# Kernel optimization log

Measured on AMD Instinct MI355X. Metric: run time of the kernel, lower is better.

The kernel has to match this reference:

```python
import jax, jax.numpy as jnp
import numpy as np

# dims
B, L, D0, P, K = 4, 512, 640, 128, 16
C, H, NL = 32, 4, 3            # hidden channels, heads, layers
DH = C // H
RAD_IN = P + 2                 # pair feat + bppm + distance
HPT = 0.3                      # high_prob_threshold


def _build_edges(bppm, coords):
    """Backbone + kNN + high-prob edges per sample, deduped, flattened over batch."""
    src_all, dst_all = [], []
    for b in range(B):
        s_bb = np.arange(L - 1); d_bb = np.arange(1, L)
        srcs = [s_bb, d_bb]; dsts = [d_bb, s_bb]
        c = coords[b]
        d2 = ((c[:, None, :] - c[None, :, :]) ** 2).sum(-1)
        nn = np.argsort(d2, axis=1)[:, 1:K + 1]            # exclude self
        s_knn = np.repeat(np.arange(L), K); d_knn = nn.reshape(-1)
        srcs += [s_knn, d_knn]; dsts += [d_knn, s_knn]
        iu, ju = np.triu_indices(L, 2)                      # |i-j| > 1
        m = bppm[b][iu, ju] >= HPT
        hs, hd = iu[m], ju[m]
        srcs += [hs, hd]; dsts += [hd, hs]
        e = np.unique(np.stack([np.concatenate(srcs), np.concatenate(dsts)], 1), axis=0)
        src_all.append(e[:, 0] + b * L); dst_all.append(e[:, 1] + b * L)
    return np.concatenate(src_all).astype(np.int32), np.concatenate(dst_all).astype(np.int32)


def setup_inputs() -> dict:
    rng = np.random.default_rng(0)
    sequence_rep = rng.standard_normal((B, L, D0)).astype(np.float32)
    pair_rep = rng.standard_normal((B, L, L, P)).astype(np.float32)
    u = rng.random((B, L, L)).astype(np.float32)
    bppm = (0.5 * (u + u.transpose(0, 2, 1))) ** 8          # sparse-ish symmetric BPPM
    initial_coords = (10.0 * rng.standard_normal((B, L, 3))).astype(np.float32)
    edge_src, edge_dst = _build_edges(bppm, initial_coords)

    def w(*shape):
        fan = shape[-2] if len(shape) >= 2 else shape[-1]
        return (rng.standard_normal(shape) / np.sqrt(fan)).astype(np.float32)

    inp = dict(
        sequence_rep=jnp.asarray(sequence_rep), pair_rep=jnp.asarray(pair_rep),
        bppm=jnp.asarray(bppm.astype(np.float32)), initial_coords=jnp.asarray(initial_coords),
        edge_src=jnp.asarray(edge_src), edge_dst=jnp.asarray(edge_dst),
        Win0=jnp.asarray(w(D0, C)), Win1=jnp.asarray(w(1, C)),
        Wr1=jnp.asarray(w(NL, RAD_IN, 64)), br1=jnp.zeros((NL, 64), jnp.float32),
        Wr2=jnp.asarray(w(NL, 64, 4 * C)), br2=jnp.zeros((NL, 4 * C), jnp.float32),
        Wm00=jnp.asarray(w(NL, C, C)), Wm01=jnp.asarray(w(NL, C, C)),
        Wm10=jnp.asarray(w(NL, C, C)), Wm11=jnp.asarray(w(NL, C, C)),
        Wq=jnp.asarray(w(NL, C, C)), Wself0=jnp.asarray(w(NL, C, C)), Wself1=jnp.asarray(w(NL, C, C)),
        gamma0=jnp.ones((NL, C), jnp.float32), beta0=jnp.zeros((NL, C), jnp.float32),
        gamma1=jnp.ones((NL, C), jnp.float32), Wout=jnp.asarray(w(C, 1)),
    )
    return inp


def _forward(sequence_rep, pair_rep, bppm, initial_coords,
             Win0, Win1, Wr1, br1, Wr2, br2, Wm00, Wm01, Wm10, Wm11,
             Wq, Wself0, Wself1, gamma0, beta0, gamma1, Wout, edge_src, edge_dst):
    N = B * L
    x = initial_coords.reshape(N, 3)
    h0 = sequence_rep.reshape(N, D0) @ Win0                  # [N,C] degree-0
    h1 = x[:, None, :] * Win1[0][None, :, None]              # [N,C,3] degree-1
    src, dst = edge_src, edge_dst
    rel = x[dst] - x[src]
    r = jnp.sqrt(jnp.sum(rel * rel, -1) + 1e-12)             # [E]
    rhat = rel / (r[:, None] + 1e-8)                         # Y1 spherical harmonic dir
    b_idx, si, di = src // L, src % L, dst % L
    ef = jnp.concatenate([pair_rep[b_idx, si, di], bppm[b_idx, si, di][:, None], r[:, None]], -1)

    for l in range(NL):
        rad = jax.nn.relu(ef @ Wr1[l] + br1[l]) @ Wr2[l] + br2[l]   # [E,4C] radial weights
        w00, w01, w10, w11 = jnp.split(rad, 4, axis=-1)
        h0s, h1s = h0[src], h1[src]
        dot1 = jnp.einsum('ecd,ed->ec', h1s, rhat)                  # deg1 -> deg0 path
        m0 = w00 * (h0s @ Wm00[l]) + w01 * (dot1 @ Wm01[l])          # [E,C]
        m1 = (w11[:, :, None] * jnp.einsum('ecd,cf->efd', h1s, Wm11[l])
              + (w10 * (h0s @ Wm10[l]))[:, :, None] * rhat[:, None, :])  # [E,C,3]
        # multi-head attention over incoming edges
        q = (h0 @ Wq[l]).reshape(N, H, DH)
        k = m0.reshape(-1, H, DH)
        logit = jnp.sum(q[dst] * k, -1) / np.sqrt(DH)                # [E,H]
        mx = jax.ops.segment_max(logit, dst, num_segments=N)
        mx = jnp.where(jnp.isfinite(mx), mx, 0.0)
        a = jnp.exp(logit - mx[dst])
        den = jax.ops.segment_sum(a, dst, num_segments=N)
        alpha = a / (den[dst] + 1e-9)                                # [E,H]
        agg0 = jax.ops.segment_sum(alpha[:, :, None] * k, dst, num_segments=N).reshape(N, C)
        agg1 = jax.ops.segment_sum(alpha[:, :, None, None] * m1.reshape(-1, H, DH, 3),
                                   dst, num_segments=N).reshape(N, C, 3)
        h0 = h0 + agg0 @ Wself0[l]
        h1 = h1 + jnp.einsum('ncd,cf->nfd', agg1, Wself1[l])
        # norms: LayerNorm on deg-0, equivariant norm-gating on deg-1
        mu = h0.mean(-1, keepdims=True)
        h0 = (h0 - mu) / jnp.sqrt(h0.var(-1, keepdims=True) + 1e-5) * gamma0[l] + beta0[l]
        nrm = jnp.sqrt(jnp.sum(h1 * h1, -1) + 1e-12)                 # [N,C]
        nln = (nrm - nrm.mean(-1, keepdims=True)) / jnp.sqrt(nrm.var(-1, keepdims=True) + 1e-5) * gamma1[l]
        h1 = h1 * (nln / (nrm + 1e-8))[:, :, None]
    delta = jnp.einsum('ncd,co->nod', h1, Wout)[:, 0, :]             # fiber_out {'1':1}
    return (x + delta).reshape(B, L, 3)


def reference(sequence_rep, pair_rep, bppm, initial_coords, edge_src, edge_dst,
              Win0, Win1, Wr1, br1, Wr2, br2, Wm00, Wm01, Wm10, Wm11,
              Wq, Wself0, Wself1, gamma0, beta0, gamma1, Wout):
    return _forward(sequence_rep, pair_rep, bppm, initial_coords,
                    Win0, Win1, Wr1, br1, Wr2, br2, Wm00, Wm01, Wm10, Wm11,
                    Wq, Wself0, Wself1, gamma0, beta0, gamma1, Wout, edge_src, edge_dst)
```

## Files before the change

kernel.cpp:

```cpp
#include <hip/hip_runtime.h>
#include <hip/hip_bf16.h>
#include <math.h>

#define BB 4
#define LL 512
#define D0 640
#define PP 128
#define CC 32
#define NLAYER 3
#define NN (BB*LL)
#define RADIN 130

typedef __attribute__((ext_vector_type(8))) short bf16x8;
typedef __attribute__((ext_vector_type(4))) float f32x4;

__device__ __forceinline__ short f2b(float v) {
    __hip_bfloat16 h = __float2bfloat16(v);
    short s; __builtin_memcpy(&s, &h, 2); return s;
}


__global__ void k_zero_int(int* __restrict__ p, int n) {
    int i = blockIdx.x * blockDim.x + threadIdx.x;
    if (i < n) p[i] = 0;
}

__global__ __launch_bounds__(64) void k_init_h0(const float* __restrict__ seq,
                                                const float* __restrict__ Win0,
                                                float* __restrict__ h0) {
    const int n = blockIdx.x, lane = threadIdx.x;
    const int c = lane & 31, half = lane >> 5;
    const float* s = seq + (size_t)n * D0;
    float acc = 0.f;
    const int i0 = half * (D0 / 2), i1 = i0 + (D0 / 2);
    for (int i = i0; i < i1; ++i) acc = fmaf(s[i], Win0[i * CC + c], acc);
    acc += __shfl_xor(acc, 32);
    if (lane < 32) h0[n * CC + c] = acc;
}

__global__ void k_init_h1(const float* __restrict__ x, const float* __restrict__ Win1,
                          float* __restrict__ h1) {
    int idx = blockIdx.x * blockDim.x + threadIdx.x;
    if (idx >= NN * CC) return;
    int n = idx >> 5, c = idx & 31;
    float w = Win1[c];
    const float* xp = x + n * 3;
    float* hp = h1 + (size_t)n * 96 + c * 3;
    hp[0] = xp[0] * w; hp[1] = xp[1] * w; hp[2] = xp[2] * w;
}

__global__ void k_geom(const int* __restrict__ src, const int* __restrict__ dst,
                       const float* __restrict__ x, float* __restrict__ r_e,
                       float* __restrict__ rhat, int E) {
    int e = blockIdx.x * blockDim.x + threadIdx.x;
    if (e >= E) return;
    int s = src[e], d = dst[e];
    float dx = x[d * 3 + 0] - x[s * 3 + 0];
    float dy = x[d * 3 + 1] - x[s * 3 + 1];
    float dz = x[d * 3 + 2] - x[s * 3 + 2];
    float r = sqrtf(dx * dx + dy * dy + dz * dz + 1e-12f);
    float ir = 1.f / (r + 1e-8f);
    r_e[e] = r;
    rhat[e * 3 + 0] = dx * ir; rhat[e * 3 + 1] = dy * ir; rhat[e * 3 + 2] = dz * ir;
}

__global__ void k_count(const int* __restrict__ dst, int* __restrict__ deg, int E) {
    int e = blockIdx.x * blockDim.x + threadIdx.x;
    if (e < E) atomicAdd(&deg[dst[e]], 1);
}

__global__ __launch_bounds__(64) void k_scan(const int* __restrict__ deg,
                                             int* __restrict__ rowptr,
                                             int* __restrict__ cursor) {
    const int lane = threadIdx.x;
    const int base = lane * 32;
    int loc[32]; int s = 0;
    for (int i = 0; i < 32; ++i) { loc[i] = deg[base + i]; s += loc[i]; }
    int pre = s;
    for (int off = 1; off < 64; off <<= 1) {
        int t = __shfl_up(pre, off);
        if (lane >= off) pre += t;
    }
    pre -= s;
    int run = pre;
    for (int i = 0; i < 32; ++i) { rowptr[base + i] = run; cursor[base + i] = 0; run += loc[i]; }
    if (lane == 63) rowptr[NN] = run;
}

__global__ void k_scatter(const int* __restrict__ dst, const int* __restrict__ rowptr,
                          int* __restrict__ cursor, int* __restrict__ eperm, int E) {
    int e = blockIdx.x * blockDim.x + threadIdx.x;
    if (e >= E) return;
    int d = dst[e];
    int pos = atomicAdd(&cursor[d], 1);
    eperm[e] = rowptr[d] + pos;
}

__global__ __launch_bounds__(256) void k_build_ef(
    const int* __restrict__ src, const int* __restrict__ dst,
    const float* __restrict__ pair, const float* __restrict__ bppm,
    const float* __restrict__ r_e, short* __restrict__ efb, int E)
{
    int e = blockIdx.x * 4 + (threadIdx.x >> 6);
    int lane = threadIdx.x & 63;
    if (e >= E) return;
    int s = src[e], d = dst[e];
    int b = s / LL, si = s % LL, di = d % LL;
    size_t prow = ((size_t)b * LL + si) * LL + di;
    const float* pr = pair + prow * PP;
    short* out = efb + (size_t)e * 160;
    out[lane] = f2b(pr[lane]);
    out[64 + lane] = f2b(pr[64 + lane]);
    if (lane < 32) {
        int idx = 128 + lane;
        float v = 0.f;
        if (idx == 128) v = bppm[prow];
        else if (idx == 129) v = r_e[e];
        out[idx] = f2b(v);
    }
}

__global__ void k_pack(const float* __restrict__ Wr1, const float* __restrict__ Wr2,
                       short* __restrict__ W1p, short* __restrict__ W2p) {
    int t = blockIdx.x * blockDim.x + threadIdx.x;
    const int tot1 = NLAYER * 5 * 4 * 64 * 8;
    const int tot2 = NLAYER * 2 * 8 * 64 * 8;
    if (t < tot1) {
        int j = t & 7; int r = t >> 3;
        int ln = r & 63; r >>= 6;
        int cb = r & 3; r >>= 2;
        int kb = r % 5; int l = r / 5;
        int row = kb * 32 + (ln >> 4) * 8 + j;
        int col = cb * 16 + (ln & 15);
        float v = (row < RADIN) ? Wr1[((size_t)l * RADIN + row) * 64 + col] : 0.f;
        W1p[t] = f2b(v);
    } else if (t < tot1 + tot2) {
        int t2 = t - tot1;
        int j = t2 & 7; int r = t2 >> 3;
        int ln = r & 63; r >>= 6;
        int cb = r & 7; r >>= 3;
        int kb = r & 1; int l = r >> 1;
        int row = kb * 32 + (ln >> 4) * 8 + j;
        int col = cb * 16 + (ln & 15);
        W2p[t2] = f2b(Wr2[((size_t)l * 64 + row) * 128 + col]);
    }
}

__global__ __launch_bounds__(256) void k_nodepre(
    int l, const float* __restrict__ h0, const float* __restrict__ h1,
    const float* __restrict__ Wq, const float* __restrict__ Wm00,
    const float* __restrict__ Wm10, const float* __restrict__ Wm11,
    float* __restrict__ qbuf, float* __restrict__ P00,
    float* __restrict__ P10, float* __restrict__ P11)
{
    __shared__ float sh0[8][32], sh1[8][96];
    const int c = threadIdx.x & 31, hw = threadIdx.x >> 5;
    const int n = blockIdx.x * 8 + hw;
    sh0[hw][c] = h0[n * CC + c];
    const float* hp = h1 + (size_t)n * 96 + c * 3;
    sh1[hw][c * 3 + 0] = hp[0]; sh1[hw][c * 3 + 1] = hp[1]; sh1[hw][c * 3 + 2] = hp[2];
    const float* WqL  = Wq   + l * 1024;
    const float* W00L = Wm00 + l * 1024;
    const float* W10L = Wm10 + l * 1024;
    const float* W11L = Wm11 + l * 1024;
    float q = 0.f, p00 = 0.f, p10 = 0.f, px = 0.f, py = 0.f, pz = 0.f;
    for (int i = 0; i < 32; ++i) {
        float a = sh0[hw][i];
        q   = fmaf(a, WqL[i * 32 + c], q);
        p00 = fmaf(a, W00L[i * 32 + c], p00);
        p10 = fmaf(a, W10L[i * 32 + c], p10);
        float w = W11L[i * 32 + c];
        px = fmaf(sh1[hw][i * 3 + 0], w, px);
        py = fmaf(sh1[hw][i * 3 + 1], w, py);
        pz = fmaf(sh1[hw][i * 3 + 2], w, pz);
    }
    qbuf[n * 32 + c] = q; P00[n * 32 + c] = p00; P10[n * 32 + c] = p10;
    float* pp = P11 + (size_t)n * 96 + c * 3;
    pp[0] = px; pp[1] = py; pp[2] = pz;
}

__global__ __launch_bounds__(256) void k_radedge(
    int l, int E,
    const int* __restrict__ src,
    const float* __restrict__ rhat,
    const short* __restrict__ efb,
    const short* __restrict__ W1p,
    const short* __restrict__ W2p,
    const float* __restrict__ br1,
    const float* __restrict__ br2,
    const float* __restrict__ Wm01,
    const float* __restrict__ h1,
    const float* __restrict__ P00,
    const float* __restrict__ P10,
    const float* __restrict__ P11,
    const int* __restrict__ eperm,
    float* __restrict__ mbuf)
{
    __shared__ short s_hid[4][16][72];
    __shared__ float s_rad[64][132];
    __shared__ float sW[1024];
    const int lane = threadIdx.x & 63, wv = threadIdx.x >> 6;
    const int r16 = lane & 15, q4 = lane >> 4;
    const int eb = blockIdx.x * 64;
    const int e0 = eb + wv * 16;

    for (int i = threadIdx.x; i < 1024; i += 256) sW[i] = Wm01[l * 1024 + i];

    f32x4 acc0 = {0.f,0.f,0.f,0.f}, acc1 = {0.f,0.f,0.f,0.f};
    f32x4 acc2 = {0.f,0.f,0.f,0.f}, acc3 = {0.f,0.f,0.f,0.f};
    int row = e0 + r16; if (row >= E) row = E - 1;
    const short* arow = efb + (size_t)row * 160 + q4 * 8;
    const short* b1b = W1p + (size_t)l * (5 * 4 * 64 * 8) + lane * 8;
    for (int kb = 0; kb < 5; ++kb) {
        bf16x8 af = *(const bf16x8*)(arow + kb * 32);
        const short* bp = b1b + kb * (4 * 64 * 8);
        bf16x8 b0 = *(const bf16x8*)(bp);
        bf16x8 b1v = *(const bf16x8*)(bp + 64 * 8);
        bf16x8 b2v = *(const bf16x8*)(bp + 2 * 64 * 8);
        bf16x8 b3v = *(const bf16x8*)(bp + 3 * 64 * 8);
        acc0 = __builtin_amdgcn_mfma_f32_16x16x32_bf16(af, b0,  acc0, 0, 0, 0);
        acc1 = __builtin_amdgcn_mfma_f32_16x16x32_bf16(af, b1v, acc1, 0, 0, 0);
        acc2 = __builtin_amdgcn_mfma_f32_16x16x32_bf16(af, b2v, acc2, 0, 0, 0);
        acc3 = __builtin_amdgcn_mfma_f32_16x16x32_bf16(af, b3v, acc3, 0, 0, 0);
    }
    {
        f32x4 a[4] = {acc0, acc1, acc2, acc3};
        for (int cb = 0; cb < 4; ++cb) {
            int col = cb * 16 + r16;
            float b = br1[l * 64 + col];
            for (int i = 0; i < 4; ++i) {
                float v = fmaxf(a[cb][i] + b, 0.f);
                s_hid[wv][q4 * 4 + i][col] = f2b(v);
            }
        }
    }
    f32x4 o[8];
    for (int cb = 0; cb < 8; ++cb) { o[cb].x=0.f; o[cb].y=0.f; o[cb].z=0.f; o[cb].w=0.f; }
    const short* b2b = W2p + (size_t)l * (2 * 8 * 64 * 8) + lane * 8;
    for (int kb = 0; kb < 2; ++kb) {
        bf16x8 af = *(const bf16x8*)(&s_hid[wv][r16][kb * 32 + q4 * 8]);
        const short* bp = b2b + kb * (8 * 64 * 8);
        for (int cb = 0; cb < 8; ++cb) {
            bf16x8 bf = *(const bf16x8*)(bp + cb * (64 * 8));
            o[cb] = __builtin_amdgcn_mfma_f32_16x16x32_bf16(af, bf, o[cb], 0, 0, 0);
        }
    }
    for (int cb = 0; cb < 8; ++cb) {
        int col = cb * 16 + r16;
        float b = br2[l * 128 + col];
        for (int i = 0; i < 4; ++i) {
            s_rad[wv * 16 + q4 * 4 + i][col] = o[cb][i] + b;
        }
    }
    __syncthreads();

    const int hw = threadIdx.x >> 5;
    const int c = lane & 31;
    const int base = lane & 32;
    for (int it = 0; it < 8; ++it) {
        const int el = hw * 8 + it;
        const int e = eb + el;
        if (e >= E) break;
        const int s = src[e];
        const float r0 = rhat[e * 3 + 0], r1 = rhat[e * 3 + 1], r2 = rhat[e * 3 + 2];
        const float* hp = h1 + (size_t)s * 96 + c * 3;
        const float dot = hp[0] * r0 + hp[1] * r1 + hp[2] * r2;
        float t1 = 0.f;
        for (int i = 0; i < 32; ++i) {
            float di = __shfl(dot, base + i);
            t1 = fmaf(di, sW[i * 32 + c], t1);
        }
        const float w00 = s_rad[el][c],      w01 = s_rad[el][32 + c];
        const float w10 = s_rad[el][64 + c], w11 = s_rad[el][96 + c];
        const float m0 = fmaf(w00, P00[s * 32 + c], w01 * t1);
        const float u10 = w10 * P10[s * 32 + c];
        const float* pp = P11 + (size_t)s * 96 + c * 3;
        float* mp = mbuf + (size_t)eperm[e] * 128;
        mp[c] = m0;
        mp[32 + c * 3 + 0] = fmaf(w11, pp[0], u10 * r0);
        mp[32 + c * 3 + 1] = fmaf(w11, pp[1], u10 * r1);
        mp[32 + c * 3 + 2] = fmaf(w11, pp[2], u10 * r2);
    }
}

__global__ __launch_bounds__(64) void k_node(
    int l, const int* __restrict__ rowptr,
    const float* __restrict__ mbuf,
    const float* __restrict__ qbuf,
    float* __restrict__ h0, float* __restrict__ h1,
    const float* __restrict__ Ws0, const float* __restrict__ Ws1,
    const float* __restrict__ gam0, const float* __restrict__ bet0,
    const float* __restrict__ gam1)
{
    const int n = blockIdx.x, lane = threadIdx.x;
    const int c = lane & 31, half = lane >> 5;
    __shared__ float s_h0[32], s_a0[32], s_a1[96];
    if (lane < 32) s_h0[lane] = h0[n * CC + lane];
    __syncthreads();

    float qc = qbuf[n * 32 + c];

    float m_run = -INFINITY, l_run = 0.f;
    float a0 = 0.f, a1x = 0.f, a1y = 0.f, a1z = 0.f;
    const int st = rowptr[n], en = rowptr[n + 1];
    for (int i = st; i < en; i += 2) {
        const int idx = i + half;
        const bool valid = idx < en;
        float kc = 0.f, mv0 = 0.f, mv1 = 0.f, mv2 = 0.f;
        if (valid) {
            const float* row = mbuf + (size_t)idx * 128;
            kc = row[c];
            mv0 = row[32 + c * 3 + 0];
            mv1 = row[32 + c * 3 + 1];
            mv2 = row[32 + c * 3 + 2];
        }
        float p = qc * kc;
        p += __shfl_xor(p, 1); p += __shfl_xor(p, 2); p += __shfl_xor(p, 4);
        if (valid) {
            float logit = p * 0.35355339059327373f;
            float mn = fmaxf(m_run, logit);
            float sc = __expf(m_run - mn);
            float w  = __expf(logit - mn);
            l_run = fmaf(l_run, sc, w);
            a0  = fmaf(a0,  sc, w * kc);
            a1x = fmaf(a1x, sc, w * mv0);
            a1y = fmaf(a1y, sc, w * mv1);
            a1z = fmaf(a1z, sc, w * mv2);
            m_run = mn;
        }
    }
    float m_o  = __shfl_xor(m_run, 32), l_o = __shfl_xor(l_run, 32);
    float a0o  = __shfl_xor(a0, 32);
    float a1xo = __shfl_xor(a1x, 32), a1yo = __shfl_xor(a1y, 32), a1zo = __shfl_xor(a1z, 32);
    float mn = fmaxf(m_run, m_o);
    float sa = 0.f, sb = 0.f;
    if (mn > -INFINITY) { sa = __expf(m_run - mn); sb = __expf(m_o - mn); }
    float den = l_run * sa + l_o * sb;
    float inv = 1.0f / (den + 1e-9f);
    float g0c = (a0  * sa + a0o  * sb) * inv;
    float g1x = (a1x * sa + a1xo * sb) * inv;
    float g1y = (a1y * sa + a1yo * sb) * inv;
    float g1z = (a1z * sa + a1zo * sb) * inv;
    if (lane < 32) {
        s_a0[c] = g0c;
        s_a1[c * 3 + 0] = g1x; s_a1[c * 3 + 1] = g1y; s_a1[c * 3 + 2] = g1z;
    }
    __syncthreads();

    float x0 = s_h0[c];
    {
        const float* W = Ws0 + l * 1024;
        for (int i = 0; i < 32; ++i) x0 = fmaf(s_a0[i], W[i * 32 + c], x0);
    }
    float mu = x0;
    mu += __shfl_xor(mu, 1); mu += __shfl_xor(mu, 2); mu += __shfl_xor(mu, 4);
    mu += __shfl_xor(mu, 8); mu += __shfl_xor(mu, 16);
    mu *= (1.f / 32.f);
    float sq = x0 * x0;
    sq += __shfl_xor(sq, 1); sq += __shfl_xor(sq, 2); sq += __shfl_xor(sq, 4);
    sq += __shfl_xor(sq, 8); sq += __shfl_xor(sq, 16);
    float var = sq * (1.f / 32.f) - mu * mu;
    float h0n = (x0 - mu) * rsqrtf(var + 1e-5f) * gam0[l * 32 + c] + bet0[l * 32 + c];
    if (lane < 32) h0[n * CC + c] = h0n;

    const float* hp = h1 + (size_t)n * 96 + c * 3;
    float v0 = hp[0], v1 = hp[1], v2 = hp[2];
    {
        const float* W = Ws1 + l * 1024;
        for (int i = 0; i < 32; ++i) {
            float w = W[i * 32 + c];
            v0 = fmaf(s_a1[i * 3 + 0], w, v0);
            v1 = fmaf(s_a1[i * 3 + 1], w, v1);
            v2 = fmaf(s_a1[i * 3 + 2], w, v2);
        }
    }
    float nrm = sqrtf(v0 * v0 + v1 * v1 + v2 * v2 + 1e-12f);
    float mu2 = nrm;
    mu2 += __shfl_xor(mu2, 1); mu2 += __shfl_xor(mu2, 2); mu2 += __shfl_xor(mu2, 4);
    mu2 += __shfl_xor(mu2, 8); mu2 += __shfl_xor(mu2, 16);
    mu2 *= (1.f / 32.f);
    float sq2 = nrm * nrm;
    sq2 += __shfl_xor(sq2, 1); sq2 += __shfl_xor(sq2, 2); sq2 += __shfl_xor(sq2, 4);
    sq2 += __shfl_xor(sq2, 8); sq2 += __shfl_xor(sq2, 16);
    float var2 = sq2 * (1.f / 32.f) - mu2 * mu2;
    float nln = (nrm - mu2) * rsqrtf(var2 + 1e-5f) * gam1[l * 32 + c];
    float scl = nln / (nrm + 1e-8f);
    if (lane < 32) {
        float* hw = h1 + (size_t)n * 96 + c * 3;
        hw[0] = v0 * scl; hw[1] = v1 * scl; hw[2] = v2 * scl;
    }
}

__global__ void k_out(const float* __restrict__ x, const float* __restrict__ h1,
                      const float* __restrict__ Wout, float* __restrict__ out) {
    int idx = blockIdx.x * blockDim.x + threadIdx.x;
    if (idx >= NN * 3) return;
    int n = idx / 3, d = idx % 3;
    float acc = x[idx];
    const float* hp = h1 + (size_t)n * 96 + d;
    for (int cc = 0; cc < 32; ++cc) acc = fmaf(hp[cc * 3], Wout[cc], acc);
    out[idx] = acc;
}

extern "C" void kernel_launch(void* const* d_in, const int* in_sizes, int n_in,
                              void* d_out, int out_size, void* d_ws, size_t ws_size,
                              hipStream_t stream) {
    const float* seq  = (const float*)d_in[0];
    const float* pair = (const float*)d_in[1];
    const float* bppm = (const float*)d_in[2];
    const float* x    = (const float*)d_in[3];
    const int*   src  = (const int*)d_in[4];
    const int*   dst  = (const int*)d_in[5];
    const float* Win0 = (const float*)d_in[6];
    const float* Win1 = (const float*)d_in[7];
    const float* Wr1  = (const float*)d_in[8];
    const float* br1  = (const float*)d_in[9];
    const float* Wr2  = (const float*)d_in[10];
    const float* br2  = (const float*)d_in[11];
    const float* Wm00 = (const float*)d_in[12];
    const float* Wm01 = (const float*)d_in[13];
    const float* Wm10 = (const float*)d_in[14];
    const float* Wm11 = (const float*)d_in[15];
    const float* Wq   = (const float*)d_in[16];
    const float* Ws0  = (const float*)d_in[17];
    const float* Ws1  = (const float*)d_in[18];
    const float* gam0 = (const float*)d_in[19];
    const float* bet0 = (const float*)d_in[20];
    const float* gam1 = (const float*)d_in[21];
    const float* Wout = (const float*)d_in[22];
    const int E = in_sizes[4];

    char* w = (char*)d_ws;
    auto alloc = [&](size_t nbytes) {
        void* p = (void*)w;
        w += (nbytes + 255) & ~(size_t)255;
        return p;
    };
    float* h0    = (float*)alloc((size_t)NN * CC * 4);
    float* h1    = (float*)alloc((size_t)NN * CC * 3 * 4);
    float* r_e   = (float*)alloc((size_t)E * 4);
    float* rhat  = (float*)alloc((size_t)E * 3 * 4);
    float* mbuf  = (float*)alloc((size_t)E * 128 * 4);
    int* deg     = (int*)alloc((size_t)NN * 4);
    int* rowptr  = (int*)alloc((size_t)(NN + 1) * 4);
    int* cursor  = (int*)alloc((size_t)NN * 4);
    int* eperm   = (int*)alloc((size_t)E * 4);
    short* efb   = (short*)alloc((size_t)E * 160 * 2);
    short* W1p   = (short*)alloc((size_t)NLAYER * 5 * 4 * 64 * 8 * 2);
    short* W2p   = (short*)alloc((size_t)NLAYER * 2 * 8 * 64 * 8 * 2);
    float* qbuf  = (float*)alloc((size_t)NN * 32 * 4);
    float* P00   = (float*)alloc((size_t)NN * 32 * 4);
    float* P10   = (float*)alloc((size_t)NN * 32 * 4);
    float* P11   = (float*)alloc((size_t)NN * 96 * 4);

    const int TB = 256;
    k_zero_int<<<(NN + TB - 1) / TB, TB, 0, stream>>>(deg, NN);
    k_init_h0<<<NN, 64, 0, stream>>>(seq, Win0, h0);
    k_init_h1<<<(NN * CC + TB - 1) / TB, TB, 0, stream>>>(x, Win1, h1);
    k_geom<<<(E + TB - 1) / TB, TB, 0, stream>>>(src, dst, x, r_e, rhat, E);
    k_count<<<(E + TB - 1) / TB, TB, 0, stream>>>(dst, deg, E);
    k_scan<<<1, 64, 0, stream>>>(deg, rowptr, cursor);
    k_scatter<<<(E + TB - 1) / TB, TB, 0, stream>>>(dst, rowptr, cursor, eperm, E);
    k_build_ef<<<(E + 3) / 4, 256, 0, stream>>>(src, dst, pair, bppm, r_e, efb, E);
    {
        int tot = NLAYER * 5 * 4 * 64 * 8 + NLAYER * 2 * 8 * 64 * 8;
        k_pack<<<(tot + TB - 1) / TB, TB, 0, stream>>>(Wr1, Wr2, W1p, W2p);
    }

    for (int l = 0; l < NLAYER; ++l) {
        k_nodepre<<<NN / 8, 256, 0, stream>>>(l, h0, h1, Wq, Wm00, Wm10, Wm11,
                                              qbuf, P00, P10, P11);
        k_radedge<<<(E + 63) / 64, 256, 0, stream>>>(l, E, src, rhat, efb, W1p, W2p,
                                                     br1, br2, Wm01, h1,
                                                     P00, P10, P11, eperm, mbuf);
        k_node<<<NN, 64, 0, stream>>>(l, rowptr, mbuf, qbuf, h0, h1,
                                      Ws0, Ws1, gam0, bet0, gam1);
    }
    k_out<<<(NN * 3 + TB - 1) / TB, TB, 0, stream>>>(x, h1, Wout, (float*)d_out);
}
```

Baseline: 855.7 us.

## Fuse edge setup kernels, widen node kernel, fold next-layer projections and output

Merges the geometry, degree counting and edge-feature build into one edge-setup kernel, and folds the degree zeroing into the h1 init kernel. The node kernel grows from 64 to 256 threads: eight half-warps each handle one edge at a time, and their online-softmax partial states are merged through shared memory. The same kernel then computes the next layer's q/P00/P10/P11 projections, or the final output projection on the last layer, so the separate k_nodepre and k_out launches inside and after the loop go away. This cuts launch count and global round-trips, at the cost of a larger node kernel with an extra shared-memory merge step and idle threads during the per-node epilogue.

```diff
diff --git a/kernel.cpp b/kernel.cpp
--- a/kernel.cpp
+++ b/kernel.cpp
@@ -19,11 +19,6 @@
     short s; __builtin_memcpy(&s, &h, 2); return s;
 }
 
-
-__global__ void k_zero_int(int* __restrict__ p, int n) {
-    int i = blockIdx.x * blockDim.x + threadIdx.x;
-    if (i < n) p[i] = 0;
-}
 
 __global__ __launch_bounds__(64) void k_init_h0(const float* __restrict__ seq,
                                                 const float* __restrict__ Win0,
@@ -39,8 +34,9 @@
 }
 
 __global__ void k_init_h1(const float* __restrict__ x, const float* __restrict__ Win1,
-                          float* __restrict__ h1) {
+                          float* __restrict__ h1, int* __restrict__ deg) {
     int idx = blockIdx.x * blockDim.x + threadIdx.x;
+    if (idx < NN) deg[idx] = 0;
     if (idx >= NN * CC) return;
     int n = idx >> 5, c = idx & 31;
     float w = Win1[c];
@@ -49,10 +45,15 @@
     hp[0] = xp[0] * w; hp[1] = xp[1] * w; hp[2] = xp[2] * w;
 }
 
-__global__ void k_geom(const int* __restrict__ src, const int* __restrict__ dst,
-                       const float* __restrict__ x, float* __restrict__ r_e,
-                       float* __restrict__ rhat, int E) {
-    int e = blockIdx.x * blockDim.x + threadIdx.x;
+__global__ __launch_bounds__(256) void k_edge_setup(
+    const int* __restrict__ src, const int* __restrict__ dst,
+    const float* __restrict__ x,
+    const float* __restrict__ pair, const float* __restrict__ bppm,
+    float* __restrict__ rhat, int* __restrict__ deg,
+    short* __restrict__ efb, int E)
+{
+    int e = blockIdx.x * 4 + (threadIdx.x >> 6);
+    int lane = threadIdx.x & 63;
     if (e >= E) return;
     int s = src[e], d = dst[e];
     float dx = x[d * 3 + 0] - x[s * 3 + 0];
@@ -60,13 +61,20 @@
     float dz = x[d * 3 + 2] - x[s * 3 + 2];
     float r = sqrtf(dx * dx + dy * dy + dz * dz + 1e-12f);
     float ir = 1.f / (r + 1e-8f);
-    r_e[e] = r;
-    rhat[e * 3 + 0] = dx * ir; rhat[e * 3 + 1] = dy * ir; rhat[e * 3 + 2] = dz * ir;
-}
-
-__global__ void k_count(const int* __restrict__ dst, int* __restrict__ deg, int E) {
-    int e = blockIdx.x * blockDim.x + threadIdx.x;
-    if (e < E) atomicAdd(&deg[dst[e]], 1);
+    int b = s / LL, si = s % LL, di = d % LL;
+    size_t prow = ((size_t)b * LL + si) * LL + di;
+    const float* pr = pair + prow * PP;
+    short* out = efb + (size_t)e * 160;
+    out[lane] = f2b(pr[lane]);
+    out[64 + lane] = f2b(pr[64 + lane]);
+    if (lane < 32) {
+        float v = 0.f;
+        if (lane == 0) v = bppm[prow];
+        else if (lane == 1) v = r;
+        out[128 + lane] = f2b(v);
+    }
+    if (lane < 3) rhat[e * 3 + lane] = (lane == 0 ? dx : lane == 1 ? dy : dz) * ir;
+    if (lane == 0) atomicAdd(&deg[d], 1);
 }
 
 __global__ __launch_bounds__(64) void k_scan(const int* __restrict__ deg,
@@ -94,30 +102,6 @@
     int d = dst[e];
     int pos = atomicAdd(&cursor[d], 1);
     eperm[e] = rowptr[d] + pos;
-}
-
-__global__ __launch_bounds__(256) void k_build_ef(
-    const int* __restrict__ src, const int* __restrict__ dst,
-    const float* __restrict__ pair, const float* __restrict__ bppm,
-    const float* __restrict__ r_e, short* __restrict__ efb, int E)
-{
-    int e = blockIdx.x * 4 + (threadIdx.x >> 6);
-    int lane = threadIdx.x & 63;
-    if (e >= E) return;
-    int s = src[e], d = dst[e];
-    int b = s / LL, si = s % LL, di = d % LL;
-    size_t prow = ((size_t)b * LL + si) * LL + di;
-    const float* pr = pair + prow * PP;
-    short* out = efb + (size_t)e * 160;
-    out[lane] = f2b(pr[lane]);
-    out[64 + lane] = f2b(pr[64 + lane]);
-    if (lane < 32) {
-        int idx = 128 + lane;
-        float v = 0.f;
-        if (idx == 128) v = bppm[prow];
-        else if (idx == 129) v = r_e[e];
-        out[idx] = f2b(v);
-    }
 }
 
 __global__ void k_pack(const float* __restrict__ Wr1, const float* __restrict__ Wr2,
@@ -283,123 +267,179 @@
     }
 }
 
-__global__ __launch_bounds__(64) void k_node(
+__global__ __launch_bounds__(256) void k_node(
     int l, const int* __restrict__ rowptr,
     const float* __restrict__ mbuf,
-    const float* __restrict__ qbuf,
+    const float* __restrict__ qbuf_in,
     float* __restrict__ h0, float* __restrict__ h1,
     const float* __restrict__ Ws0, const float* __restrict__ Ws1,
     const float* __restrict__ gam0, const float* __restrict__ bet0,
-    const float* __restrict__ gam1)
+    const float* __restrict__ gam1,
+    const float* __restrict__ Wq, const float* __restrict__ Wm00,
+    const float* __restrict__ Wm10, const float* __restrict__ Wm11,
+    float* __restrict__ qout, float* __restrict__ P00,
+    float* __restrict__ P10, float* __restrict__ P11,
+    const float* __restrict__ x, const float* __restrict__ Wout,
+    float* __restrict__ outp)
 {
-    const int n = blockIdx.x, lane = threadIdx.x;
-    const int c = lane & 31, half = lane >> 5;
-    __shared__ float s_h0[32], s_a0[32], s_a1[96];
-    if (lane < 32) s_h0[lane] = h0[n * CC + lane];
-    __syncthreads();
-
-    float qc = qbuf[n * 32 + c];
+    const int n = blockIdx.x;
+    const int tid = threadIdx.x;
+    const int hw = tid >> 5;
+    const int c = tid & 31;
+    __shared__ float s_part[8][32][6];
+    __shared__ float s_a0[32], s_a1[96];
+    __shared__ float s_hn[128];
+
+    const float qc = qbuf_in[n * 32 + c];
+    const int st = rowptr[n], en = rowptr[n + 1];
 
     float m_run = -INFINITY, l_run = 0.f;
     float a0 = 0.f, a1x = 0.f, a1y = 0.f, a1z = 0.f;
-    const int st = rowptr[n], en = rowptr[n + 1];
-    for (int i = st; i < en; i += 2) {
-        const int idx = i + half;
-        const bool valid = idx < en;
-        float kc = 0.f, mv0 = 0.f, mv1 = 0.f, mv2 = 0.f;
-        if (valid) {
-            const float* row = mbuf + (size_t)idx * 128;
-            kc = row[c];
-            mv0 = row[32 + c * 3 + 0];
-            mv1 = row[32 + c * 3 + 1];
-            mv2 = row[32 + c * 3 + 2];
-        }
+    for (int idx = st + hw; idx < en; idx += 8) {
+        const float* row = mbuf + (size_t)idx * 128;
+        const float kc = row[c];
+        const float mv0 = row[32 + c * 3 + 0];
+        const float mv1 = row[32 + c * 3 + 1];
+        const float mv2 = row[32 + c * 3 + 2];
         float p = qc * kc;
         p += __shfl_xor(p, 1); p += __shfl_xor(p, 2); p += __shfl_xor(p, 4);
-        if (valid) {
-            float logit = p * 0.35355339059327373f;
-            float mn = fmaxf(m_run, logit);
-            float sc = __expf(m_run - mn);
-            float w  = __expf(logit - mn);
-            l_run = fmaf(l_run, sc, w);
-            a0  = fmaf(a0,  sc, w * kc);
-            a1x = fmaf(a1x, sc, w * mv0);
-            a1y = fmaf(a1y, sc, w * mv1);
-            a1z = fmaf(a1z, sc, w * mv2);
-            m_run = mn;
-        }
-    }
-    float m_o  = __shfl_xor(m_run, 32), l_o = __shfl_xor(l_run, 32);
-    float a0o  = __shfl_xor(a0, 32);
-    float a1xo = __shfl_xor(a1x, 32), a1yo = __shfl_xor(a1y, 32), a1zo = __shfl_xor(a1z, 32);
-    float mn = fmaxf(m_run, m_o);
-    float sa = 0.f, sb = 0.f;
-    if (mn > -INFINITY) { sa = __expf(m_run - mn); sb = __expf(m_o - mn); }
-    float den = l_run * sa + l_o * sb;
-    float inv = 1.0f / (den + 1e-9f);
-    float g0c = (a0  * sa + a0o  * sb) * inv;
-    float g1x = (a1x * sa + a1xo * sb) * inv;
-    float g1y = (a1y * sa + a1yo * sb) * inv;
-    float g1z = (a1z * sa + a1zo * sb) * inv;
-    if (lane < 32) {
-        s_a0[c] = g0c;
-        s_a1[c * 3 + 0] = g1x; s_a1[c * 3 + 1] = g1y; s_a1[c * 3 + 2] = g1z;
-    }
+        const float logit = p * 0.35355339059327373f;
+        const float mn = fmaxf(m_run, logit);
+        const float sc = __expf(m_run - mn);
+        const float w  = __expf(logit - mn);
+        l_run = fmaf(l_run, sc, w);
+        a0  = fmaf(a0,  sc, w * kc);
+        a1x = fmaf(a1x, sc, w * mv0);
+        a1y = fmaf(a1y, sc, w * mv1);
+        a1z = fmaf(a1z, sc, w * mv2);
+        m_run = mn;
+    }
+    s_part[hw][c][0] = m_run; s_part[hw][c][1] = l_run;
+    s_part[hw][c][2] = a0;
+    s_part[hw][c][3] = a1x; s_part[hw][c][4] = a1y; s_part[hw][c][5] = a1z;
     __syncthreads();
 
-    float x0 = s_h0[c];
-    {
-        const float* W = Ws0 + l * 1024;
-        for (int i = 0; i < 32; ++i) x0 = fmaf(s_a0[i], W[i * 32 + c], x0);
-    }
-    float mu = x0;
-    mu += __shfl_xor(mu, 1); mu += __shfl_xor(mu, 2); mu += __shfl_xor(mu, 4);
-    mu += __shfl_xor(mu, 8); mu += __shfl_xor(mu, 16);
-    mu *= (1.f / 32.f);
-    float sq = x0 * x0;
-    sq += __shfl_xor(sq, 1); sq += __shfl_xor(sq, 2); sq += __shfl_xor(sq, 4);
-    sq += __shfl_xor(sq, 8); sq += __shfl_xor(sq, 16);
-    float var = sq * (1.f / 32.f) - mu * mu;
-    float h0n = (x0 - mu) * rsqrtf(var + 1e-5f) * gam0[l * 32 + c] + bet0[l * 32 + c];
-    if (lane < 32) h0[n * CC + c] = h0n;
-
-    const float* hp = h1 + (size_t)n * 96 + c * 3;
-    float v0 = hp[0], v1 = hp[1], v2 = hp[2];
-    {
-        const float* W = Ws1 + l * 1024;
-        for (int i = 0; i < 32; ++i) {
-            float w = W[i * 32 + c];
-            v0 = fmaf(s_a1[i * 3 + 0], w, v0);
-            v1 = fmaf(s_a1[i * 3 + 1], w, v1);
-            v2 = fmaf(s_a1[i * 3 + 2], w, v2);
-        }
-    }
-    float nrm = sqrtf(v0 * v0 + v1 * v1 + v2 * v2 + 1e-12f);
-    float mu2 = nrm;
-    mu2 += __shfl_xor(mu2, 1); mu2 += __shfl_xor(mu2, 2); mu2 += __shfl_xor(mu2, 4);
-    mu2 += __shfl_xor(mu2, 8); mu2 += __shfl_xor(mu2, 16);
-    mu2 *= (1.f / 32.f);
-    float sq2 = nrm * nrm;
-    sq2 += __shfl_xor(sq2, 1); sq2 += __shfl_xor(sq2, 2); sq2 += __shfl_xor(sq2, 4);
-    sq2 += __shfl_xor(sq2, 8); sq2 += __shfl_xor(sq2, 16);
-    float var2 = sq2 * (1.f / 32.f) - mu2 * mu2;
-    float nln = (nrm - mu2) * rsqrtf(var2 + 1e-5f) * gam1[l * 32 + c];
-    float scl = nln / (nrm + 1e-8f);
-    if (lane < 32) {
-        float* hw = h1 + (size_t)n * 96 + c * 3;
-        hw[0] = v0 * scl; hw[1] = v1 * scl; hw[2] = v2 * scl;
-    }
-}
-
-__global__ void k_out(const float* __restrict__ x, const float* __restrict__ h1,
-                      const float* __restrict__ Wout, float* __restrict__ out) {
-    int idx = blockIdx.x * blockDim.x + threadIdx.x;
-    if (idx >= NN * 3) return;
-    int n = idx / 3, d = idx % 3;
-    float acc = x[idx];
-    const float* hp = h1 + (size_t)n * 96 + d;
-    for (int cc = 0; cc < 32; ++cc) acc = fmaf(hp[cc * 3], Wout[cc], acc);
-    out[idx] = acc;
+    if (tid < 32) {
+        float M = s_part[0][c][0], L = s_part[0][c][1], A0 = s_part[0][c][2];
+        float Ax = s_part[0][c][3], Ay = s_part[0][c][4], Az = s_part[0][c][5];
+        for (int k = 1; k < 8; ++k) {
+            const float m2 = s_part[k][c][0];
+            if (m2 == -INFINITY) continue;
+            const float mn = fmaxf(M, m2);
+            const float sa = (M == -INFINITY) ? 0.f : __expf(M - mn);
+            const float sb = __expf(m2 - mn);
+            L  = L  * sa + s_part[k][c][1] * sb;
+            A0 = A0 * sa + s_part[k][c][2] * sb;
+            Ax = Ax * sa + s_part[k][c][3] * sb;
+            Ay = Ay * sa + s_part[k][c][4] * sb;
+            Az = Az * sa + s_part[k][c][5] * sb;
+            M = mn;
+        }
+        const float inv = 1.0f / (L + 1e-9f);
+        s_a0[c] = A0 * inv;
+        s_a1[c * 3 + 0] = Ax * inv;
+        s_a1[c * 3 + 1] = Ay * inv;
+        s_a1[c * 3 + 2] = Az * inv;
+    }
+    __syncthreads();
+
+    if (tid < 32) {
+        float x0 = h0[n * CC + c];
+        {
+            const float* W = Ws0 + l * 1024;
+            for (int i = 0; i < 32; ++i) x0 = fmaf(s_a0[i], W[i * 32 + c], x0);
+        }
+        float mu = x0;
+        mu += __shfl_xor(mu, 1); mu += __shfl_xor(mu, 2); mu += __shfl_xor(mu, 4);
+        mu += __shfl_xor(mu, 8); mu += __shfl_xor(mu, 16);
+        mu *= (1.f / 32.f);
+        float sq = x0 * x0;
+        sq += __shfl_xor(sq, 1); sq += __shfl_xor(sq, 2); sq += __shfl_xor(sq, 4);
+        sq += __shfl_xor(sq, 8); sq += __shfl_xor(sq, 16);
+        float var = sq * (1.f / 32.f) - mu * mu;
+        float h0n = (x0 - mu) * rsqrtf(var + 1e-5f) * gam0[l * 32 + c] + bet0[l * 32 + c];
+        s_hn[c] = h0n;
+        if (l + 1 < NLAYER) h0[n * CC + c] = h0n;
+
+        const float* hp = h1 + (size_t)n * 96 + c * 3;
+        float v0 = hp[0], v1 = hp[1], v2 = hp[2];
+        {
+            const float* W = Ws1 + l * 1024;
+            for (int i = 0; i < 32; ++i) {
+                float w = W[i * 32 + c];
+                v0 = fmaf(s_a1[i * 3 + 0], w, v0);
+                v1 = fmaf(s_a1[i * 3 + 1], w, v1);
+                v2 = fmaf(s_a1[i * 3 + 2], w, v2);
+            }
+        }
+        float nrm = sqrtf(v0 * v0 + v1 * v1 + v2 * v2 + 1e-12f);
+        float mu2 = nrm;
+        mu2 += __shfl_xor(mu2, 1); mu2 += __shfl_xor(mu2, 2); mu2 += __shfl_xor(mu2, 4);
+        mu2 += __shfl_xor(mu2, 8); mu2 += __shfl_xor(mu2, 16);
+        mu2 *= (1.f / 32.f);
+        float sq2 = nrm * nrm;
+        sq2 += __shfl_xor(sq2, 1); sq2 += __shfl_xor(sq2, 2); sq2 += __shfl_xor(sq2, 4);
+        sq2 += __shfl_xor(sq2, 8); sq2 += __shfl_xor(sq2, 16);
+        float var2 = sq2 * (1.f / 32.f) - mu2 * mu2;
+        float nln = (nrm - mu2) * rsqrtf(var2 + 1e-5f) * gam1[l * 32 + c];
+        float scl = nln / (nrm + 1e-8f);
+        float w0 = v0 * scl, w1 = v1 * scl, w2 = v2 * scl;
+        s_hn[32 + c * 3 + 0] = w0;
+        s_hn[32 + c * 3 + 1] = w1;
+        s_hn[32 + c * 3 + 2] = w2;
+        if (l + 1 < NLAYER) {
+            float* hq = h1 + (size_t)n * 96 + c * 3;
+            hq[0] = w0; hq[1] = w1; hq[2] = w2;
+        } else {
+            const float wo = Wout[c];
+            float d0 = w0 * wo, d1 = w1 * wo, d2 = w2 * wo;
+            d0 += __shfl_xor(d0, 1); d1 += __shfl_xor(d1, 1); d2 += __shfl_xor(d2, 1);
+            d0 += __shfl_xor(d0, 2); d1 += __shfl_xor(d1, 2); d2 += __shfl_xor(d2, 2);
+            d0 += __shfl_xor(d0, 4); d1 += __shfl_xor(d1, 4); d2 += __shfl_xor(d2, 4);
+            d0 += __shfl_xor(d0, 8); d1 += __shfl_xor(d1, 8); d2 += __shfl_xor(d2, 8);
+            d0 += __shfl_xor(d0, 16); d1 += __shfl_xor(d1, 16); d2 += __shfl_xor(d2, 16);
+            if (c == 0) {
+                outp[n * 3 + 0] = x[n * 3 + 0] + d0;
+                outp[n * 3 + 1] = x[n * 3 + 1] + d1;
+                outp[n * 3 + 2] = x[n * 3 + 2] + d2;
+            }
+        }
+    }
+
+    if (l + 1 < NLAYER) {
+        __syncthreads();
+        const int grp = tid >> 5;
+        if (grp < 4) {
+            const int lp = l + 1;
+            if (grp == 0) {
+                const float* W = Wq + lp * 1024;
+                float acc = 0.f;
+                for (int i = 0; i < 32; ++i) acc = fmaf(s_hn[i], W[i * 32 + c], acc);
+                qout[n * 32 + c] = acc;
+            } else if (grp == 1) {
+                const float* W = Wm00 + lp * 1024;
+                float acc = 0.f;
+                for (int i = 0; i < 32; ++i) acc = fmaf(s_hn[i], W[i * 32 + c], acc);
+                P00[n * 32 + c] = acc;
+            } else if (grp == 2) {
+                const float* W = Wm10 + lp * 1024;
+                float acc = 0.f;
+                for (int i = 0; i < 32; ++i) acc = fmaf(s_hn[i], W[i * 32 + c], acc);
+                P10[n * 32 + c] = acc;
+            } else {
+                const float* W = Wm11 + lp * 1024;
+                float px = 0.f, py = 0.f, pz = 0.f;
+                for (int i = 0; i < 32; ++i) {
+                    float w = W[i * 32 + c];
+                    px = fmaf(s_hn[32 + i * 3 + 0], w, px);
+                    py = fmaf(s_hn[32 + i * 3 + 1], w, py);
+                    pz = fmaf(s_hn[32 + i * 3 + 2], w, pz);
+                }
+                float* pp = P11 + (size_t)n * 96 + c * 3;
+                pp[0] = px; pp[1] = py; pp[2] = pz;
+            }
+        }
+    }
 }
 
 extern "C" void kernel_launch(void* const* d_in, const int* in_sizes, int n_in,
@@ -438,7 +478,6 @@
     };
     float* h0    = (float*)alloc((size_t)NN * CC * 4);
     float* h1    = (float*)alloc((size_t)NN * CC * 3 * 4);
-    float* r_e   = (float*)alloc((size_t)E * 4);
     float* rhat  = (float*)alloc((size_t)E * 3 * 4);
     float* mbuf  = (float*)alloc((size_t)E * 128 * 4);
     int* deg     = (int*)alloc((size_t)NN * 4);
@@ -454,27 +493,27 @@
     float* P11   = (float*)alloc((size_t)NN * 96 * 4);
 
     const int TB = 256;
-    k_zero_int<<<(NN + TB - 1) / TB, TB, 0, stream>>>(deg, NN);
     k_init_h0<<<NN, 64, 0, stream>>>(seq, Win0, h0);
-    k_init_h1<<<(NN * CC + TB - 1) / TB, TB, 0, stream>>>(x, Win1, h1);
-    k_geom<<<(E + TB - 1) / TB, TB, 0, stream>>>(src, dst, x, r_e, rhat, E);
-    k_count<<<(E + TB - 1) / TB, TB, 0, stream>>>(dst, deg, E);
+    k_init_h1<<<(NN * CC + TB - 1) / TB, TB, 0, stream>>>(x, Win1, h1, deg);
+    k_edge_setup<<<(E + 3) / 4, 256, 0, stream>>>(src, dst, x, pair, bppm,
+                                                  rhat, deg, efb, E);
     k_scan<<<1, 64, 0, stream>>>(deg, rowptr, cursor);
     k_scatter<<<(E + TB - 1) / TB, TB, 0, stream>>>(dst, rowptr, cursor, eperm, E);
-    k_build_ef<<<(E + 3) / 4, 256, 0, stream>>>(src, dst, pair, bppm, r_e, efb, E);
     {
         int tot = NLAYER * 5 * 4 * 64 * 8 + NLAYER * 2 * 8 * 64 * 8;
         k_pack<<<(tot + TB - 1) / TB, TB, 0, stream>>>(Wr1, Wr2, W1p, W2p);
     }
+    k_nodepre<<<NN / 8, 256, 0, stream>>>(0, h0, h1, Wq, Wm00, Wm10, Wm11,
+                                          qbuf, P00, P10, P11);
 
     for (int l = 0; l < NLAYER; ++l) {
-        k_nodepre<<<NN / 8, 256, 0, stream>>>(l, h0, h1, Wq, Wm00, Wm10, Wm11,
-                                              qbuf, P00, P10, P11);
         k_radedge<<<(E + 63) / 64, 256, 0, stream>>>(l, E, src, rhat, efb, W1p, W2p,
                                                      br1, br2, Wm01, h1,
                                                      P00, P10, P11, eperm, mbuf);
-        k_node<<<NN, 64, 0, stream>>>(l, rowptr, mbuf, qbuf, h0, h1,
-                                      Ws0, Ws1, gam0, bet0, gam1);
-    }
-    k_out<<<(NN * 3 + TB - 1) / TB, TB, 0, stream>>>(x, h1, Wout, (float*)d_out);
-}
+        k_node<<<NN, 256, 0, stream>>>(l, rowptr, mbuf, qbuf, h0, h1,
+                                       Ws0, Ws1, gam0, bet0, gam1,
+                                       Wq, Wm00, Wm10, Wm11,
+                                       qbuf, P00, P10, P11,
+                                       x, Wout, (float*)d_out);
+    }
+}
```

Result: faster. 837.1 us (-2.2%).
